# Performance work log

Hardware: AMD Instinct MI355X
Metric: run time of the kernel (lower is better)

## Reference

```python
import jax, jax.numpy as jnp
import numpy as np

# QuadFittingFromFlow: per-pixel quadratic least-squares fit from flow.
# The CUDA extension source is unavailable; this reference implements the
# standard per-pixel quadratic cost-surface fit it describes:
#  1. for each pixel p, bilinearly sample feat1 at p + flow + (ox,oy) for the
#     3x3 offset grid (ox,oy in {-1,0,1}) and compute the SSD matching cost
#     against feat0(p)  -> 9 cost samples c_k per pixel.
#  2. fit a 2D quadratic c(x,y) ~ a x^2 + b y^2 + c xy + d x + e y + f by
#     (softmin-)weighted least squares, solving the per-pixel 6x6 normal
#     equations. Output sol = the 6 quadratic coefficients per pixel (Y,X,6).
# The 3rd flow channel (validity/confidence) does not alter the LS solution
# (uniform per-pixel rescaling of weights) and is ignored, matching the
# module's docstring that only 2 displacement channels matter.

Y, X, L = 384, 512, 32
EPS = 1e-4  # Tikhonov regularization for the 6x6 solve

# fixed 3x3 offset grid and quadratic design matrix A (9 samples x 6 coeffs)
_oy, _ox = np.meshgrid(np.arange(-1, 2), np.arange(-1, 2), indexing='ij')
OFFS_X = jnp.asarray(_ox.reshape(-1), dtype=jnp.float32)  # (9,)
OFFS_Y = jnp.asarray(_oy.reshape(-1), dtype=jnp.float32)  # (9,)
_A = np.stack([_ox.reshape(-1) ** 2, _oy.reshape(-1) ** 2,
               _ox.reshape(-1) * _oy.reshape(-1),
               _ox.reshape(-1), _oy.reshape(-1),
               np.ones(9)], axis=1).astype(np.float32)
A_DESIGN = jnp.asarray(_A)  # (9, 6)


def _bilinear(feat, px, py):
    # feat: (Y,X,L); px,py: (Y,X,9) fractional sample coords -> (Y,X,9,L)
    Yd, Xd, _ = feat.shape
    x0f, y0f = jnp.floor(px), jnp.floor(py)
    wx = (px - x0f)[..., None]
    wy = (py - y0f)[..., None]
    x0 = jnp.clip(x0f.astype(jnp.int32), 0, Xd - 1)
    x1 = jnp.clip(x0 + 1, 0, Xd - 1)
    y0 = jnp.clip(y0f.astype(jnp.int32), 0, Yd - 1)
    y1 = jnp.clip(y0 + 1, 0, Yd - 1)
    f00 = feat[y0, x0]
    f01 = feat[y0, x1]
    f10 = feat[y1, x0]
    f11 = feat[y1, x1]
    return (f00 * (1 - wx) * (1 - wy) + f01 * wx * (1 - wy)
            + f10 * (1 - wx) * wy + f11 * wx * wy)


def _quadfit(t_feat0, t_feat1, t_flow):
    Yd, Xd, _ = t_feat0.shape
    u, v = t_flow[..., 0], t_flow[..., 1]  # displacement channels
    gy, gx = jnp.meshgrid(jnp.arange(Yd, dtype=jnp.float32),
                          jnp.arange(Xd, dtype=jnp.float32), indexing='ij')
    px = gx[..., None] + u[..., None] + OFFS_X  # (Y,X,9)
    py = gy[..., None] + v[..., None] + OFFS_Y
    samp = _bilinear(t_feat1, px, py)           # (Y,X,9,L)
    c = jnp.sum((t_feat0[:, :, None, :] - samp) ** 2, axis=-1)  # (Y,X,9)
    w = jax.nn.softmax(-c, axis=-1)             # robust per-pixel weights
    AtWA = jnp.einsum('ki,yxk,kj->yxij', A_DESIGN, w, A_DESIGN) \
        + EPS * jnp.eye(6, dtype=t_feat0.dtype)  # (Y,X,6,6)
    rhs = jnp.einsum('ki,yxk->yxi', A_DESIGN, w * c)  # (Y,X,6)
    sol = jnp.linalg.solve(AtWA, rhs[..., None])[..., 0]
    return sol  # (Y,X,6)


def setup_inputs() -> dict:
    key = jax.random.key(0)
    k0, k1, k2 = jax.random.split(key, 3)
    t_feat0 = jax.random.normal(k0, (Y, X, L), dtype=jnp.float32)
    t_feat1 = jax.random.normal(k1, (Y, X, L), dtype=jnp.float32)
    t_flow = jax.random.normal(k2, (Y, X, 3), dtype=jnp.float32) * 2.0
    return {"t_feat0": t_feat0, "t_feat1": t_feat1, "t_flow": t_flow}


def reference(t_feat0, t_feat1, t_flow):
    return _quadfit(t_feat0, t_feat1, t_flow)
```

## Files before the change

kernel.cpp:

```cpp
#include <hip/hip_runtime.h>
#include <math.h>

#define Ydim 384
#define Xdim 512
#define NPIX (Ydim * Xdim)
#define EPS 1e-4

__device__ __forceinline__ double fast_rcp64(double d) {
    double r = (double)__builtin_amdgcn_rcpf((float)d);
    r = r * (2.0 - d * r);
    r = r * (2.0 - d * r);
    return r;
}

__global__ __launch_bounds__(256) void qf_fused_kernel(
    const float* __restrict__ feat0,
    const float* __restrict__ feat1,
    const float* __restrict__ flow,
    float* __restrict__ out)
{
    __shared__ float cost_lds[32 * 9];

    const int t   = threadIdx.x;
    const int g   = t >> 3;
    const int sub = t & 7;
    const int pix = blockIdx.x * 32 + g;
    const int y = pix >> 9;
    const int x = pix & (Xdim - 1);

    const float u = flow[pix * 3 + 0];
    const float v = flow[pix * 3 + 1];
    const float4 f0 = *(const float4*)(feat0 + (size_t)pix * 32 + sub * 4);

    const float pxc = (float)x + u;
    const float pyc = (float)y + v;

    int   c0[3], c1[3], r0[3], r1[3];
    float wx[3], wy[3];
#pragma unroll
    for (int j = 0; j < 3; ++j) {
        float px = pxc + (float)(j - 1);
        float fx = floorf(px);
        wx[j] = px - fx;
        int xi = min(max((int)fx, 0), Xdim - 1);
        c0[j] = xi;
        c1[j] = min(xi + 1, Xdim - 1);
        float py = pyc + (float)(j - 1);
        float fy = floorf(py);
        wy[j] = py - fy;
        int yi = min(max((int)fy, 0), Ydim - 1);
        r0[j] = yi;
        r1[j] = min(yi + 1, Ydim - 1);
    }

    float cacc[9];
    const bool fast = (c1[0] == c0[1]) & (c1[1] == c0[2])
                    & (r1[0] == r0[1]) & (r1[1] == r0[2]);

    if (fast) {
        const int cols[4] = {c0[0], c0[1], c0[2], c1[2]};
        const int rows[4] = {r0[0], r0[1], r0[2], r1[2]};
        float4 F[4][4];
#pragma unroll
        for (int r = 0; r < 4; ++r) {
            const float* rb = feat1 + ((size_t)rows[r] * Xdim) * 32 + sub * 4;
#pragma unroll
            for (int c = 0; c < 4; ++c)
                F[r][c] = *(const float4*)(rb + (size_t)cols[c] * 32);
        }
#pragma unroll
        for (int i = 0; i < 3; ++i) {
            float wyv = wy[i], omwy = 1.f - wyv;
#pragma unroll
            for (int j = 0; j < 3; ++j) {
                float wxv = wx[j], omwx = 1.f - wxv;
                float w00 = omwx * omwy, w01 = wxv * omwy;
                float w10 = omwx * wyv,  w11 = wxv * wyv;
                float4 a = F[i][j], b = F[i][j + 1], c = F[i + 1][j], d = F[i + 1][j + 1];
                float dx = f0.x - (a.x * w00 + b.x * w01 + c.x * w10 + d.x * w11);
                float dy = f0.y - (a.y * w00 + b.y * w01 + c.y * w10 + d.y * w11);
                float dz = f0.z - (a.z * w00 + b.z * w01 + c.z * w10 + d.z * w11);
                float dw = f0.w - (a.w * w00 + b.w * w01 + c.w * w10 + d.w * w11);
                cacc[i * 3 + j] = dx * dx + dy * dy + dz * dz + dw * dw;
            }
        }
    } else {
#pragma unroll
        for (int i = 0; i < 3; ++i) {
            float wyv = wy[i], omwy = 1.f - wyv;
            int rb0 = r0[i] * (Xdim * 32);
            int rb1 = r1[i] * (Xdim * 32);
#pragma unroll
            for (int j = 0; j < 3; ++j) {
                const float4 f00 = *(const float4*)(feat1 + rb0 + c0[j] * 32 + sub * 4);
                const float4 f01 = *(const float4*)(feat1 + rb0 + c1[j] * 32 + sub * 4);
                const float4 f10 = *(const float4*)(feat1 + rb1 + c0[j] * 32 + sub * 4);
                const float4 f11 = *(const float4*)(feat1 + rb1 + c1[j] * 32 + sub * 4);
                float wxv = wx[j], omwx = 1.f - wxv;
                float w00 = omwx * omwy, w01 = wxv * omwy;
                float w10 = omwx * wyv,  w11 = wxv * wyv;
                float dx = f0.x - (f00.x * w00 + f01.x * w01 + f10.x * w10 + f11.x * w11);
                float dy = f0.y - (f00.y * w00 + f01.y * w01 + f10.y * w10 + f11.y * w11);
                float dz = f0.z - (f00.z * w00 + f01.z * w01 + f10.z * w10 + f11.z * w11);
                float dw = f0.w - (f00.w * w00 + f01.w * w01 + f10.w * w10 + f11.w * w11);
                cacc[i * 3 + j] = dx * dx + dy * dy + dz * dz + dw * dw;
            }
        }
    }

#pragma unroll
    for (int m = 1; m <= 4; m <<= 1) {
#pragma unroll
        for (int k = 0; k < 9; ++k)
            cacc[k] += __shfl_xor(cacc[k], m);
    }
    if (sub == 0) {
#pragma unroll
        for (int k = 0; k < 9; ++k)
            cost_lds[g * 9 + k] = cacc[k];
    }
    __syncthreads();

    if (t >= 32) return;

    float c[9];
#pragma unroll
    for (int k = 0; k < 9; ++k) c[k] = cost_lds[t * 9 + k];

    float cmin = c[0];
#pragma unroll
    for (int k = 1; k < 9; ++k) cmin = fminf(cmin, c[k]);

    float e[9], sumf = 0.f;
#pragma unroll
    for (int k = 0; k < 9; ++k) {
        e[k] = expf(cmin - c[k]);
        sumf += e[k];
    }
    float invs = 1.f / sumf;

    float w[9], q[9];
#pragma unroll
    for (int k = 0; k < 9; ++k) {
        w[k] = e[k] * invs;
        q[k] = w[k] * c[k];
    }

    float sc0 = w[0] + w[3] + w[6], sc2 = w[2] + w[5] + w[8];
    float sr0 = w[0] + w[1] + w[2], sr2 = w[6] + w[7] + w[8];
    float S10 = sc2 - sc0, S20 = sc2 + sc0;
    float S01 = sr2 - sr0, S02 = sr2 + sr0;
    float S11 = (w[0] + w[8]) - (w[2] + w[6]);
    float S21 = (w[6] + w[8]) - (w[0] + w[2]);
    float S12 = (w[2] + w[8]) - (w[0] + w[6]);
    float S22 = w[0] + w[2] + w[6] + w[8];
    float S00 = sr0 + w[3] + w[4] + w[5] + sr2;

    float qc0 = q[0] + q[3] + q[6], qc2 = q[2] + q[5] + q[8];
    float qr0 = q[0] + q[1] + q[2], qr2 = q[6] + q[7] + q[8];
    float T10 = qc2 - qc0, T20 = qc2 + qc0;
    float T01 = qr2 - qr0, T02 = qr2 + qr0;
    float T11 = (q[0] + q[8]) - (q[2] + q[6]);
    float T00 = qr0 + q[3] + q[4] + q[5] + qr2;

    double M[6][6], rhs[6], ip[6];
    M[0][0] = (double)S20 + EPS; M[0][1] = S22; M[0][2] = S11; M[0][3] = S10; M[0][4] = S21; M[0][5] = S20;
    M[1][1] = (double)S02 + EPS; M[1][2] = S11; M[1][3] = S12; M[1][4] = S01; M[1][5] = S02;
    M[2][2] = (double)S22 + EPS; M[2][3] = S21; M[2][4] = S12; M[2][5] = S11;
    M[3][3] = (double)S20 + EPS; M[3][4] = S11; M[3][5] = S10;
    M[4][4] = (double)S02 + EPS; M[4][5] = S01;
    M[5][5] = (double)S00 + EPS;
    rhs[0] = T20; rhs[1] = T02; rhs[2] = T11; rhs[3] = T10; rhs[4] = T01; rhs[5] = T00;

#pragma unroll
    for (int p = 0; p < 6; ++p) {
        ip[p] = fast_rcp64(M[p][p]);
#pragma unroll
        for (int r = p + 1; r < 6; ++r) {
            double f = M[p][r] * ip[p];
#pragma unroll
            for (int cc = r; cc < 6; ++cc)
                M[r][cc] -= f * M[p][cc];
            rhs[r] -= f * rhs[p];
        }
    }
    double sol[6];
#pragma unroll
    for (int p = 5; p >= 0; --p) {
        double s2 = rhs[p];
#pragma unroll
        for (int cc = p + 1; cc < 6; ++cc) s2 -= M[p][cc] * sol[cc];
        sol[p] = s2 * ip[p];
    }

    const int opix = blockIdx.x * 32 + t;
#pragma unroll
    for (int i = 0; i < 6; ++i) out[(size_t)opix * 6 + i] = (float)sol[i];
}

extern "C" void kernel_launch(void* const* d_in, const int* in_sizes, int n_in,
                              void* d_out, int out_size, void* d_ws, size_t ws_size,
                              hipStream_t stream) {
    const float* feat0 = (const float*)d_in[0];
    const float* feat1 = (const float*)d_in[1];
    const float* flow  = (const float*)d_in[2];
    float* out = (float*)d_out;

    qf_fused_kernel<<<dim3(NPIX / 32), dim3(256), 0, stream>>>(feat0, feat1, flow, out);
}
```

Baseline: 109.6 us.

## Solve 6x6 system in fp32 LU with fp64 iterative refinement; enlarge blocks

Replaces the fully fp64 Gaussian elimination with an fp32 LU factorisation and triangular solves, then runs one step of iterative refinement whose residual is computed in fp64. This moves most of the solve off the much slower fp64 path while trying to keep accuracy close to the double-precision result. Blocks double to 512 threads covering 64 pixels, so 64 lanes run the solve tail instead of 32. The tail is still serial per pixel, and larger blocks mean more threads idle at the barrier.

```diff
diff --git a/kernel.cpp b/kernel.cpp
--- a/kernel.cpp
+++ b/kernel.cpp
@@ -4,27 +4,26 @@
 #define Ydim 384
 #define Xdim 512
 #define NPIX (Ydim * Xdim)
-#define EPS 1e-4
-
-__device__ __forceinline__ double fast_rcp64(double d) {
-    double r = (double)__builtin_amdgcn_rcpf((float)d);
-    r = r * (2.0 - d * r);
-    r = r * (2.0 - d * r);
+#define EPS 1e-4f
+
+__device__ __forceinline__ float fast_rcp32(float d) {
+    float r = __builtin_amdgcn_rcpf(d);
+    r = r * (2.f - d * r);
     return r;
 }
 
-__global__ __launch_bounds__(256) void qf_fused_kernel(
+__global__ __launch_bounds__(512, 4) void qf_fused_kernel(
     const float* __restrict__ feat0,
     const float* __restrict__ feat1,
     const float* __restrict__ flow,
     float* __restrict__ out)
 {
-    __shared__ float cost_lds[32 * 9];
+    __shared__ float cost_lds[64 * 9];
 
     const int t   = threadIdx.x;
     const int g   = t >> 3;
     const int sub = t & 7;
-    const int pix = blockIdx.x * 32 + g;
+    const int pix = blockIdx.x * 64 + g;
     const int y = pix >> 9;
     const int x = pix & (Xdim - 1);
 
@@ -76,11 +75,11 @@
                 float wxv = wx[j], omwx = 1.f - wxv;
                 float w00 = omwx * omwy, w01 = wxv * omwy;
                 float w10 = omwx * wyv,  w11 = wxv * wyv;
-                float4 a = F[i][j], b = F[i][j + 1], c = F[i + 1][j], d = F[i + 1][j + 1];
-                float dx = f0.x - (a.x * w00 + b.x * w01 + c.x * w10 + d.x * w11);
-                float dy = f0.y - (a.y * w00 + b.y * w01 + c.y * w10 + d.y * w11);
-                float dz = f0.z - (a.z * w00 + b.z * w01 + c.z * w10 + d.z * w11);
-                float dw = f0.w - (a.w * w00 + b.w * w01 + c.w * w10 + d.w * w11);
+                float4 a = F[i][j], bb = F[i][j + 1], c = F[i + 1][j], d = F[i + 1][j + 1];
+                float dx = f0.x - (a.x * w00 + bb.x * w01 + c.x * w10 + d.x * w11);
+                float dy = f0.y - (a.y * w00 + bb.y * w01 + c.y * w10 + d.y * w11);
+                float dz = f0.z - (a.z * w00 + bb.z * w01 + c.z * w10 + d.z * w11);
+                float dw = f0.w - (a.w * w00 + bb.w * w01 + c.w * w10 + d.w * w11);
                 cacc[i * 3 + j] = dx * dx + dy * dy + dz * dz + dw * dw;
             }
         }
@@ -121,7 +120,7 @@
     }
     __syncthreads();
 
-    if (t >= 32) return;
+    if (t >= 64) return;
 
     float c[9];
 #pragma unroll
@@ -137,7 +136,8 @@
         e[k] = expf(cmin - c[k]);
         sumf += e[k];
     }
-    float invs = 1.f / sumf;
+    float invs = fast_rcp32(sumf);
+    invs = invs * (2.f - sumf * invs);
 
     float w[9], q[9];
 #pragma unroll
@@ -163,39 +163,76 @@
     float T11 = (q[0] + q[8]) - (q[2] + q[6]);
     float T00 = qr0 + q[3] + q[4] + q[5] + qr2;
 
-    double M[6][6], rhs[6], ip[6];
-    M[0][0] = (double)S20 + EPS; M[0][1] = S22; M[0][2] = S11; M[0][3] = S10; M[0][4] = S21; M[0][5] = S20;
-    M[1][1] = (double)S02 + EPS; M[1][2] = S11; M[1][3] = S12; M[1][4] = S01; M[1][5] = S02;
-    M[2][2] = (double)S22 + EPS; M[2][3] = S21; M[2][4] = S12; M[2][5] = S11;
-    M[3][3] = (double)S20 + EPS; M[3][4] = S11; M[3][5] = S10;
-    M[4][4] = (double)S02 + EPS; M[4][5] = S01;
-    M[5][5] = (double)S00 + EPS;
-    rhs[0] = T20; rhs[1] = T02; rhs[2] = T11; rhs[3] = T10; rhs[4] = T01; rhs[5] = T00;
-
+    float M[6][6];
+    M[0][0] = S20 + EPS; M[0][1] = S22; M[0][2] = S11; M[0][3] = S10; M[0][4] = S21; M[0][5] = S20;
+    M[1][0] = S22; M[1][1] = S02 + EPS; M[1][2] = S11; M[1][3] = S12; M[1][4] = S01; M[1][5] = S02;
+    M[2][0] = S11; M[2][1] = S11; M[2][2] = S22 + EPS; M[2][3] = S21; M[2][4] = S12; M[2][5] = S11;
+    M[3][0] = S10; M[3][1] = S12; M[3][2] = S21; M[3][3] = S20 + EPS; M[3][4] = S11; M[3][5] = S10;
+    M[4][0] = S21; M[4][1] = S01; M[4][2] = S12; M[4][3] = S11; M[4][4] = S02 + EPS; M[4][5] = S01;
+    M[5][0] = S20; M[5][1] = S02; M[5][2] = S11; M[5][3] = S10; M[5][4] = S01; M[5][5] = S00 + EPS;
+    float rhs[6] = {T20, T02, T11, T10, T01, T00};
+
+    float ip[6];
 #pragma unroll
     for (int p = 0; p < 6; ++p) {
-        ip[p] = fast_rcp64(M[p][p]);
+        ip[p] = fast_rcp32(M[p][p]);
 #pragma unroll
         for (int r = p + 1; r < 6; ++r) {
-            double f = M[p][r] * ip[p];
-#pragma unroll
-            for (int cc = r; cc < 6; ++cc)
+            float f = M[r][p] * ip[p];
+            M[r][p] = f;
+#pragma unroll
+            for (int cc = p + 1; cc < 6; ++cc)
                 M[r][cc] -= f * M[p][cc];
-            rhs[r] -= f * rhs[p];
-        }
-    }
-    double sol[6];
+        }
+    }
+
+    float s[6];
+#pragma unroll
+    for (int p = 0; p < 6; ++p) {
+        float tt = rhs[p];
+#pragma unroll
+        for (int j = 0; j < 6; ++j) if (j < p) tt -= M[p][j] * s[j];
+        s[p] = tt;
+    }
 #pragma unroll
     for (int p = 5; p >= 0; --p) {
-        double s2 = rhs[p];
-#pragma unroll
-        for (int cc = p + 1; cc < 6; ++cc) s2 -= M[p][cc] * sol[cc];
-        sol[p] = s2 * ip[p];
-    }
-
-    const int opix = blockIdx.x * 32 + t;
-#pragma unroll
-    for (int i = 0; i < 6; ++i) out[(size_t)opix * 6 + i] = (float)sol[i];
+        float tt = s[p];
+#pragma unroll
+        for (int j = 0; j < 6; ++j) if (j > p) tt -= M[p][j] * s[j];
+        s[p] = tt * ip[p];
+    }
+
+    double s0 = s[0], s1 = s[1], s2 = s[2], s3 = s[3], s4 = s[4], s5 = s[5];
+    double dS20 = S20, dS02 = S02, dS22 = S22, dS11 = S11, dS10 = S10,
+           dS01 = S01, dS21 = S21, dS12 = S12, dS00 = S00, dE = (double)EPS;
+    double rd[6];
+    rd[0] = (double)T20 - ((dS20 + dE) * s0 + dS22 * s1 + dS11 * s2 + dS10 * s3 + dS21 * s4 + dS20 * s5);
+    rd[1] = (double)T02 - (dS22 * s0 + (dS02 + dE) * s1 + dS11 * s2 + dS12 * s3 + dS01 * s4 + dS02 * s5);
+    rd[2] = (double)T11 - (dS11 * s0 + dS11 * s1 + (dS22 + dE) * s2 + dS21 * s3 + dS12 * s4 + dS11 * s5);
+    rd[3] = (double)T10 - (dS10 * s0 + dS12 * s1 + dS21 * s2 + (dS20 + dE) * s3 + dS11 * s4 + dS10 * s5);
+    rd[4] = (double)T01 - (dS21 * s0 + dS01 * s1 + dS12 * s2 + dS11 * s3 + (dS02 + dE) * s4 + dS01 * s5);
+    rd[5] = (double)T00 - (dS20 * s0 + dS02 * s1 + dS11 * s2 + dS10 * s3 + dS01 * s4 + (dS00 + dE) * s5);
+
+    float d[6];
+#pragma unroll
+    for (int p = 0; p < 6; ++p) {
+        float tt = (float)rd[p];
+#pragma unroll
+        for (int j = 0; j < 6; ++j) if (j < p) tt -= M[p][j] * d[j];
+        d[p] = tt;
+    }
+#pragma unroll
+    for (int p = 5; p >= 0; --p) {
+        float tt = d[p];
+#pragma unroll
+        for (int j = 0; j < 6; ++j) if (j > p) tt -= M[p][j] * d[j];
+        d[p] = tt * ip[p];
+    }
+
+    const int opix = blockIdx.x * 64 + t;
+#pragma unroll
+    for (int i = 0; i < 6; ++i)
+        out[(size_t)opix * 6 + i] = s[i] + d[i];
 }
 
 extern "C" void kernel_launch(void* const* d_in, const int* in_sizes, int n_in,
@@ -206,5 +243,5 @@
     const float* flow  = (const float*)d_in[2];
     float* out = (float*)d_out;
 
-    qf_fused_kernel<<<dim3(NPIX / 32), dim3(256), 0, stream>>>(feat0, feat1, flow, out);
+    qf_fused_kernel<<<dim3(NPIX / 64), dim3(512), 0, stream>>>(feat0, feat1, flow, out);
 }
```

After: 111.1 us. No clear change (+1.4%).
